# Kernel tuning notes

Hardware: AMD Instinct MI355X
Metric: run time of the kernel (lower is better)

## Reference

```python
import jax, jax.numpy as jnp
import numpy as np
import math

NM = 1024
NH = 16
ND = NM // NH
B, L = 4, 1024


def setup_inputs() -> dict:
    key = jax.random.key(0)
    ks = jax.random.split(key, 11)
    s = 1.0 / math.sqrt(NM)
    return {
        "x": jax.random.normal(ks[0], (B, L, NM), dtype=jnp.float32),
        "mask": jax.random.randint(ks[1], (B, L, L), 0, 2, dtype=jnp.int32),
        "Wq": jax.random.normal(ks[2], (NM, NM), dtype=jnp.float32) * s,
        "bq": jax.random.normal(ks[3], (NM,), dtype=jnp.float32) * 0.01,
        "Wk": jax.random.normal(ks[4], (NM, NM), dtype=jnp.float32) * s,
        "bk": jax.random.normal(ks[5], (NM,), dtype=jnp.float32) * 0.01,
        "Wv": jax.random.normal(ks[6], (NM, NM), dtype=jnp.float32) * s,
        "bv": jax.random.normal(ks[7], (NM,), dtype=jnp.float32) * 0.01,
        "Wo": jax.random.normal(ks[8], (NM, NM), dtype=jnp.float32) * s,
        "bo": jax.random.normal(ks[9], (NM,), dtype=jnp.float32) * 0.01,
    }


def reference(x, mask, Wq, bq, Wk, bk, Wv, bv, Wo, bo):
    nB, nL, _ = x.shape
    m = mask.astype(x.dtype)  # [B,L,L]
    # QKV projections (torch Linear: y = x @ W.T + b)
    q = (x @ Wq.T + bq).reshape(nB, nL, NH, ND)
    k = (x @ Wk.T + bk).reshape(nB, nL, NH, ND)
    v = (x @ Wv.T + bv).reshape(nB, nL, NH, ND)
    # scaled dot product; NOTE: module scales by 1/sqrt(nM), not 1/sqrt(nD)
    scores = jnp.einsum("bqhd,bkhd->bhqk", q, k) / math.sqrt(NM)
    # additive/multiplicative padding mask: S*mask - (1-mask)*1e9
    mb = m[:, None, :, :]  # broadcast over heads [B,1,L,L]
    scores = scores * mb - (1.0 - mb) * 1e9
    attn = jax.nn.softmax(scores, axis=-1)
    ctx = jnp.einsum("bhqk,bkhd->bqhd", attn, v).reshape(nB, nL, NM)
    out = ctx @ Wo.T + bo
    return out
```

## Files before the change

kernel.cpp:

```cpp
#include <hip/hip_runtime.h>

typedef unsigned short u16;
typedef unsigned int   u32;
typedef unsigned long long u64;
typedef __attribute__((ext_vector_type(8))) short    short8;
typedef __attribute__((ext_vector_type(4))) float    floatx4;
typedef __attribute__((ext_vector_type(4))) _Float16 half4v;
typedef __attribute__((ext_vector_type(8))) _Float16 half8v;

#define NM 1024
#define NH 16
#define ND 64
#define BB 4
#define LL 1024
#define MM (BB*LL)

__device__ __forceinline__ u16 f2bf(float f) {
  union { float f; u32 u; } c; c.f = f;
  u32 u = c.u;
  return (u16)((u + 0x7fffu + ((u >> 16) & 1u)) >> 16);
}

__device__ __forceinline__ void cstore(u16* p, float v)  { *p = f2bf(v); }
__device__ __forceinline__ void cstore(float* p, float v){ *p = v; }

__device__ __forceinline__ void load_lds16(const void* g, void* l) {
  __builtin_amdgcn_global_load_lds((const __attribute__((address_space(1))) u32*)g,
                                   (__attribute__((address_space(3))) u32*)l,
                                   16, 0, 0);
}

__device__ __forceinline__ int vperm(int K) {
  return (K & ~31) | (((K >> 2) & 3) << 3) | (((K >> 4) & 1) << 2) | (K & 3);
}

__global__ void conv_all(const float* __restrict__ x,  const float* __restrict__ Wq,
                         const float* __restrict__ Wk, const float* __restrict__ Wv,
                         const float* __restrict__ Wo, const int* __restrict__ m,
                         u16* __restrict__ xb, u16* __restrict__ wcat,
                         u16* __restrict__ wob, u32* __restrict__ mp) {
  const int y = blockIdx.y;
  const int base = blockIdx.x * 256 + threadIdx.x;
  if (y == 5) {
    const int lane = threadIdx.x & 63;
    #pragma unroll
    for (int t = 0; t < 16; t++) {
      int i = base + t * 262144;
      int v = m[i];
      u64 bits = __ballot(v != 0);
      if (lane == 0) {
        mp[(i >> 5) + 0] = (u32)bits;
        mp[(i >> 5) + 1] = (u32)(bits >> 32);
      }
    }
    return;
  }
  const float* src; u16* dst;
  if      (y == 0) { src = x;  dst = xb; }
  else if (y == 1) { src = Wq; dst = wcat; }
  else if (y == 2) { src = Wk; dst = wcat + NM * NM; }
  else if (y == 3) { src = Wv; dst = wcat + 2 * NM * NM; }
  else             { src = Wo; dst = wob; }
  const int nrep = (y == 0) ? 4 : 1;
  for (int t = 0; t < nrep; t++) {
    int i = (base + t * 262144) * 4;
    float4 v = *(const float4*)(src + i);
    ushort4 o;
    o.x = f2bf(v.x); o.y = f2bf(v.y); o.z = f2bf(v.z); o.w = f2bf(v.w);
    *(ushort4*)(dst + i) = o;
  }
}

template<int TM, int TN, typename OUT_T, bool TRANS_Z2>
__global__ __launch_bounds__(256)
void gemm_bt_kernel(const u16* __restrict__ A,
                    const u16* __restrict__ Ball,
                    const float* __restrict__ b0, const float* __restrict__ b1,
                    const float* __restrict__ b2,
                    OUT_T* __restrict__ Call,
                    _Float16* __restrict__ VTout)
{
  constexpr int K = 1024, N = 1024;
  constexpr int NI = TM / 32, NJ = TN / 32;
  constexpr int CH = (TM + TN) / 16;
  const int z = blockIdx.z;
  const u16* Bm = Ball + (size_t)z * N * K;
  const float* bias = (z == 0) ? b0 : ((z == 1) ? b1 : b2);
  OUT_T* C = Call + (size_t)z * MM * N;

  __shared__ u16 S[(TM + TN) * 32];
  u16* As = S;
  u16* Bs = S + TM * 32;

  const int tid = threadIdx.x;
  const int w = tid >> 6, lane = tid & 63, lane15 = lane & 15, quad = lane >> 4;
  const int row0 = blockIdx.x * TM, col0 = blockIdx.y * TN;
  const int wm = (w >> 1) * (TM / 2), wn = (w & 1) * (TN / 2);
  const int sr = lane >> 2, sc = (lane & 3) * 8;

  floatx4 acc[NI][NJ];
  const floatx4 zero = {0.f, 0.f, 0.f, 0.f};
  #pragma unroll
  for (int i = 0; i < NI; i++)
    #pragma unroll
    for (int j = 0; j < NJ; j++) acc[i][j] = zero;

  for (int kk = 0; kk < K; kk += 32) {
    __syncthreads();
    #pragma unroll
    for (int c = 0; c < CH / 4; c++) {
      int g = w * (CH / 4) + c;
      const u16* src;
      if (g * 16 < TM) src = A  + (size_t)(row0 + g * 16 + sr) * K + kk + sc;
      else             src = Bm + (size_t)(col0 + (g * 16 - TM) + sr) * K + kk + sc;
      load_lds16(src, &S[g * 512]);
    }
    __syncthreads();

    short8 af[NI], bf[NJ];
    #pragma unroll
    for (int i = 0; i < NI; i++)
      af[i] = *(short8*)&As[(wm + i * 16 + lane15) * 32 + quad * 8];
    #pragma unroll
    for (int j = 0; j < NJ; j++)
      bf[j] = *(short8*)&Bs[(wn + j * 16 + lane15) * 32 + quad * 8];
    #pragma unroll
    for (int i = 0; i < NI; i++)
      #pragma unroll
      for (int j = 0; j < NJ; j++)
        acc[i][j] = __builtin_amdgcn_mfma_f32_16x16x32_bf16(af[i], bf[j], acc[i][j], 0, 0, 0);
  }

  #pragma unroll
  for (int i = 0; i < NI; i++) {
    #pragma unroll
    for (int j = 0; j < NJ; j++) {
      int col = col0 + wn + j * 16 + lane15;
      float bv = bias[col];
      if (TRANS_Z2 && z == 2) {
        int row = row0 + wm + i * 16 + quad * 4;
        int Kk = row & (LL - 1), bb = row & ~(LL - 1);
        int o = vperm(Kk);
        half4v hv;
        hv.x = (_Float16)(acc[i][j][0] + bv);
        hv.y = (_Float16)(acc[i][j][1] + bv);
        hv.z = (_Float16)(acc[i][j][2] + bv);
        hv.w = (_Float16)(acc[i][j][3] + bv);
        *(half4v*)&VTout[(size_t)col * MM + bb + o] = hv;
      } else {
        #pragma unroll
        for (int r = 0; r < 4; r++) {
          int row = row0 + wm + i * 16 + quad * 4 + r;
          cstore(&C[(size_t)row * N + col], acc[i][j][r] + bv);
        }
      }
    }
  }
}

__global__ __launch_bounds__(256, 2)
void attn_kernel(const u16* __restrict__ Q, const u16* __restrict__ K,
                 const _Float16* __restrict__ VT, const u32* __restrict__ mp,
                 u16* __restrict__ CTX)
{
  __shared__ u16      Ks[2 * 128 * 32];
  __shared__ _Float16 Vs[64 * 128];

  const int tid = threadIdx.x;
  const int w = tid >> 6, lane = tid & 63, lane15 = lane & 15, quad = lane >> 4;
  const int qb = blockIdx.x * 128, bh = blockIdx.y;
  const int b = bh >> 4, h = bh & 15;
  const size_t kvbase = (size_t)(b * LL) * NM + h * ND;
  const size_t vtbase = (size_t)(h * ND) * MM + (size_t)b * LL;
  const float scale = 0.03125f;

  int q0g[2];
  q0g[0] = qb + w * 16;
  q0g[1] = qb + 64 + w * 16;

  short8 aq[2][2];
  #pragma unroll
  for (int g = 0; g < 2; g++) {
    const u16* qp = Q + (size_t)(b * LL + q0g[g] + lane15) * NM + h * ND + quad * 8;
    aq[g][0] = *(const short8*)(qp);
    aq[g][1] = *(const short8*)(qp + 32);
  }

  const int ksrow = lane >> 2;
  const int kscg  = (lane & 3) ^ (ksrow & 3);
  const int vsd   = lane >> 4;
  const int vscg  = (lane & 15);

  const floatx4 zero = {0.f, 0.f, 0.f, 0.f};
  floatx4 o_acc[2][4] = {{zero, zero, zero, zero}, {zero, zero, zero, zero}};
  float lsum[2] = {0.f, 0.f};

  const u32* mrow0 = mp + (size_t)(b * LL + q0g[0] + lane15) * 32;
  const u32* mrow1 = mp + (size_t)(b * LL + q0g[1] + lane15) * 32;

  #pragma unroll 1
  for (int kt = 0; kt < 8; kt++) {
    const int k0 = kt * 128;

    __syncthreads();
    #pragma unroll
    for (int t = 0; t < 4; t++) {
      int n = w * 4 + t;
      int s = n & 1, r0 = (n >> 1) * 16;
      int row = r0 + ksrow;
      load_lds16(K + kvbase + (size_t)(k0 + row) * NM + s * 32 + kscg * 8,
                 &Ks[n * 512]);
    }
    #pragma unroll
    for (int t = 0; t < 4; t++) {
      int n = w * 4 + t;
      int d = n * 4 + vsd;
      int cg = vscg ^ (d & 15);
      load_lds16(VT + vtbase + (size_t)d * MM + k0 + cg * 8, &Vs[n * 512]);
    }
    __syncthreads();

    #pragma unroll
    for (int g = 0; g < 2; g++) {
      const u32* mrow = g ? mrow1 : mrow0;
      const uint4 m4 = *(const uint4*)(mrow + kt * 4);

      half4v pf[8];
      #pragma unroll
      for (int j = 0; j < 8; j++) {
        const int ch = (quad ^ (lane15 & 3)) * 8;
        const int kbase = j * 1024 + lane15 * 32 + ch;
        const short8 kf0 = *(const short8*)&Ks[kbase];
        const short8 kf1 = *(const short8*)&Ks[kbase + 512];
        floatx4 sT = zero;
        sT = __builtin_amdgcn_mfma_f32_16x16x32_bf16(kf0, aq[g][0], sT, 0, 0, 0);
        sT = __builtin_amdgcn_mfma_f32_16x16x32_bf16(kf1, aq[g][1], sT, 0, 0, 0);
        const u32 mw = (j & 2) ? ((j & 4) ? m4.w : m4.y) : ((j & 4) ? m4.z : m4.x);
        const int sh = (j & 1) * 16 + quad * 4;
        float p[4];
        #pragma unroll
        for (int r = 0; r < 4; r++) {
          float e = __expf(sT[r] * scale);
          p[r] = ((mw >> (sh + r)) & 1u) ? e : 0.f;
          lsum[g] += p[r];
        }
        const auto lo = __builtin_amdgcn_cvt_pkrtz(p[0], p[1]);
        const auto hi = __builtin_amdgcn_cvt_pkrtz(p[2], p[3]);
        half4v pj;
        pj.x = (_Float16)lo.x; pj.y = (_Float16)lo.y;
        pj.z = (_Float16)hi.x; pj.w = (_Float16)hi.y;
        pf[j] = pj;
      }

      #pragma unroll
      for (int jd = 0; jd < 4; jd++) {
        const int d = jd * 16 + lane15;
        #pragma unroll
        for (int j2 = 0; j2 < 4; j2++) {
          const int cidx = (j2 * 4 + quad) ^ (d & 15);
          const half8v vv = *(const half8v*)&Vs[d * 128 + cidx * 8];
          const half4v vlo = __builtin_shufflevector(vv, vv, 0, 1, 2, 3);
          const half4v vhi = __builtin_shufflevector(vv, vv, 4, 5, 6, 7);
          o_acc[g][jd] = __builtin_amdgcn_mfma_f32_16x16x16f16(vlo, pf[2 * j2],     o_acc[g][jd], 0, 0, 0);
          o_acc[g][jd] = __builtin_amdgcn_mfma_f32_16x16x16f16(vhi, pf[2 * j2 + 1], o_acc[g][jd], 0, 0, 0);
        }
      }
    }
  }

  #pragma unroll
  for (int g = 0; g < 2; g++) {
    float ls = lsum[g];
    ls += __shfl_xor(ls, 16);
    ls += __shfl_xor(ls, 32);
    const float inv = 1.0f / ls;
    const size_t obase = (size_t)(b * LL + q0g[g] + lane15) * NM + h * ND;
    #pragma unroll
    for (int jd = 0; jd < 4; jd++) {
      ushort4 o;
      o.x = f2bf(o_acc[g][jd][0] * inv);
      o.y = f2bf(o_acc[g][jd][1] * inv);
      o.z = f2bf(o_acc[g][jd][2] * inv);
      o.w = f2bf(o_acc[g][jd][3] * inv);
      *(ushort4*)(CTX + obase + jd * 16 + quad * 4) = o;
    }
  }
}

extern "C" void kernel_launch(void* const* d_in, const int* in_sizes, int n_in,
                              void* d_out, int out_size, void* d_ws, size_t ws_size,
                              hipStream_t stream) {
  const float* x  = (const float*)d_in[0];
  const int*   mk = (const int*)  d_in[1];
  const float* Wq = (const float*)d_in[2]; const float* bq = (const float*)d_in[3];
  const float* Wk = (const float*)d_in[4]; const float* bk = (const float*)d_in[5];
  const float* Wv = (const float*)d_in[6]; const float* bv = (const float*)d_in[7];
  const float* Wo = (const float*)d_in[8]; const float* bo = (const float*)d_in[9];
  float* out = (float*)d_out;

  char* ws = (char*)d_ws;
  u16* xb        = (u16*)(ws);
  u16* Wcat      = (u16*)(ws + ((size_t)8  << 20));
  u16* Wob       = (u16*)(ws + ((size_t)14 << 20));
  u16* QKb       = (u16*)(ws + ((size_t)16 << 20));
  _Float16* VT   = (_Float16*)(ws + ((size_t)32 << 20));
  u16* CTX       = (u16*)(ws + ((size_t)40 << 20));
  u32* mp        = (u32*)(ws + ((size_t)48 << 20));

  conv_all<<<dim3(1024, 6), 256, 0, stream>>>(x, Wq, Wk, Wv, Wo, mk,
                                              xb, Wcat, Wob, mp);

  gemm_bt_kernel<128, 128, u16, true><<<dim3(32, 8, 3), 256, 0, stream>>>(
      xb, Wcat, bq, bk, bv, QKb, VT);

  attn_kernel<<<dim3(8, 64), 256, 0, stream>>>(
      QKb, QKb + (size_t)MM * NM, VT, mp, CTX);

  gemm_bt_kernel<64, 128, float, false><<<dim3(64, 8, 1), 256, 0, stream>>>(
      CTX, Wob, bo, bo, bo, out, nullptr);
}
```

Before: 198.1 us.

## Double GEMM K-step to 64 and fuse attention query groups with 16x16x32 f16 MFMA

```diff
diff --git a/kernel.cpp b/kernel.cpp
--- a/kernel.cpp
+++ b/kernel.cpp
@@ -82,15 +82,13 @@
 {
   constexpr int K = 1024, N = 1024;
   constexpr int NI = TM / 32, NJ = TN / 32;
-  constexpr int CH = (TM + TN) / 16;
+  constexpr int CH = (TM + TN) / 8;
   const int z = blockIdx.z;
   const u16* Bm = Ball + (size_t)z * N * K;
   const float* bias = (z == 0) ? b0 : ((z == 1) ? b1 : b2);
   OUT_T* C = Call + (size_t)z * MM * N;
 
-  __shared__ u16 S[(TM + TN) * 32];
-  u16* As = S;
-  u16* Bs = S + TM * 32;
+  __shared__ u16 S[(TM + TN) * 64];
 
   const int tid = threadIdx.x;
   const int w = tid >> 6, lane = tid & 63, lane15 = lane & 15, quad = lane >> 4;
@@ -105,30 +103,35 @@
     #pragma unroll
     for (int j = 0; j < NJ; j++) acc[i][j] = zero;
 
-  for (int kk = 0; kk < K; kk += 32) {
+  for (int kk = 0; kk < K; kk += 64) {
     __syncthreads();
     #pragma unroll
     for (int c = 0; c < CH / 4; c++) {
       int g = w * (CH / 4) + c;
+      int rg = g >> 1, s = g & 1;
+      int grow = rg * 16 + sr;
       const u16* src;
-      if (g * 16 < TM) src = A  + (size_t)(row0 + g * 16 + sr) * K + kk + sc;
-      else             src = Bm + (size_t)(col0 + (g * 16 - TM) + sr) * K + kk + sc;
+      if (grow < TM) src = A  + (size_t)(row0 + grow) * K + kk + s * 32 + sc;
+      else           src = Bm + (size_t)(col0 + grow - TM) * K + kk + s * 32 + sc;
       load_lds16(src, &S[g * 512]);
     }
     __syncthreads();
 
-    short8 af[NI], bf[NJ];
-    #pragma unroll
-    for (int i = 0; i < NI; i++)
-      af[i] = *(short8*)&As[(wm + i * 16 + lane15) * 32 + quad * 8];
-    #pragma unroll
-    for (int j = 0; j < NJ; j++)
-      bf[j] = *(short8*)&Bs[(wn + j * 16 + lane15) * 32 + quad * 8];
-    #pragma unroll
-    for (int i = 0; i < NI; i++)
+    #pragma unroll
+    for (int s = 0; s < 2; s++) {
+      short8 af[NI], bf[NJ];
+      #pragma unroll
+      for (int i = 0; i < NI; i++)
+        af[i] = *(short8*)&S[((wm >> 4) + i) * 1024 + s * 512 + lane15 * 32 + quad * 8];
       #pragma unroll
       for (int j = 0; j < NJ; j++)
-        acc[i][j] = __builtin_amdgcn_mfma_f32_16x16x32_bf16(af[i], bf[j], acc[i][j], 0, 0, 0);
+        bf[j] = *(short8*)&S[(((TM + wn) >> 4) + j) * 1024 + s * 512 + lane15 * 32 + quad * 8];
+      #pragma unroll
+      for (int i = 0; i < NI; i++)
+        #pragma unroll
+        for (int j = 0; j < NJ; j++)
+          acc[i][j] = __builtin_amdgcn_mfma_f32_16x16x32_bf16(af[i], bf[j], acc[i][j], 0, 0, 0);
+    }
   }
 
   #pragma unroll
@@ -201,6 +204,9 @@
   #pragma unroll 1
   for (int kt = 0; kt < 8; kt++) {
     const int k0 = kt * 128;
+    uint4 m4g[2];
+    m4g[0] = *(const uint4*)(mrow0 + kt * 4);
+    m4g[1] = *(const uint4*)(mrow1 + kt * 4);
 
     __syncthreads();
     #pragma unroll
@@ -220,27 +226,27 @@
     }
     __syncthreads();
 
-    #pragma unroll
-    for (int g = 0; g < 2; g++) {
-      const u32* mrow = g ? mrow1 : mrow0;
-      const uint4 m4 = *(const uint4*)(mrow + kt * 4);
-
-      half4v pf[8];
-      #pragma unroll
-      for (int j = 0; j < 8; j++) {
-        const int ch = (quad ^ (lane15 & 3)) * 8;
-        const int kbase = j * 1024 + lane15 * 32 + ch;
-        const short8 kf0 = *(const short8*)&Ks[kbase];
-        const short8 kf1 = *(const short8*)&Ks[kbase + 512];
-        floatx4 sT = zero;
-        sT = __builtin_amdgcn_mfma_f32_16x16x32_bf16(kf0, aq[g][0], sT, 0, 0, 0);
-        sT = __builtin_amdgcn_mfma_f32_16x16x32_bf16(kf1, aq[g][1], sT, 0, 0, 0);
+    half4v pf[2][8];
+    #pragma unroll
+    for (int j = 0; j < 8; j++) {
+      const int ch = (quad ^ (lane15 & 3)) * 8;
+      const int kbase = j * 1024 + lane15 * 32 + ch;
+      const short8 kf0 = *(const short8*)&Ks[kbase];
+      const short8 kf1 = *(const short8*)&Ks[kbase + 512];
+      floatx4 sT[2];
+      sT[0] = __builtin_amdgcn_mfma_f32_16x16x32_bf16(kf0, aq[0][0], zero, 0, 0, 0);
+      sT[1] = __builtin_amdgcn_mfma_f32_16x16x32_bf16(kf0, aq[1][0], zero, 0, 0, 0);
+      sT[0] = __builtin_amdgcn_mfma_f32_16x16x32_bf16(kf1, aq[0][1], sT[0], 0, 0, 0);
+      sT[1] = __builtin_amdgcn_mfma_f32_16x16x32_bf16(kf1, aq[1][1], sT[1], 0, 0, 0);
+      const int sh = (j & 1) * 16 + quad * 4;
+      #pragma unroll
+      for (int g = 0; g < 2; g++) {
+        const uint4 m4 = m4g[g];
         const u32 mw = (j & 2) ? ((j & 4) ? m4.w : m4.y) : ((j & 4) ? m4.z : m4.x);
-        const int sh = (j & 1) * 16 + quad * 4;
         float p[4];
         #pragma unroll
         for (int r = 0; r < 4; r++) {
-          float e = __expf(sT[r] * scale);
+          float e = __expf(sT[g][r] * scale);
           p[r] = ((mw >> (sh + r)) & 1u) ? e : 0.f;
           lsum[g] += p[r];
         }
@@ -249,21 +255,23 @@
         half4v pj;
         pj.x = (_Float16)lo.x; pj.y = (_Float16)lo.y;
         pj.z = (_Float16)hi.x; pj.w = (_Float16)hi.y;
-        pf[j] = pj;
+        pf[g][j] = pj;
       }
-
+    }
+
+    #pragma unroll
+    for (int t = 0; t < 4; t++) {
+      const half8v b80 = __builtin_shufflevector(pf[0][2 * t], pf[0][2 * t + 1],
+                                                 0, 1, 2, 3, 4, 5, 6, 7);
+      const half8v b81 = __builtin_shufflevector(pf[1][2 * t], pf[1][2 * t + 1],
+                                                 0, 1, 2, 3, 4, 5, 6, 7);
       #pragma unroll
       for (int jd = 0; jd < 4; jd++) {
         const int d = jd * 16 + lane15;
-        #pragma unroll
-        for (int j2 = 0; j2 < 4; j2++) {
-          const int cidx = (j2 * 4 + quad) ^ (d & 15);
-          const half8v vv = *(const half8v*)&Vs[d * 128 + cidx * 8];
-          const half4v vlo = __builtin_shufflevector(vv, vv, 0, 1, 2, 3);
-          const half4v vhi = __builtin_shufflevector(vv, vv, 4, 5, 6, 7);
-          o_acc[g][jd] = __builtin_amdgcn_mfma_f32_16x16x16f16(vlo, pf[2 * j2],     o_acc[g][jd], 0, 0, 0);
-          o_acc[g][jd] = __builtin_amdgcn_mfma_f32_16x16x16f16(vhi, pf[2 * j2 + 1], o_acc[g][jd], 0, 0, 0);
-        }
+        const int cidx = (t * 4 + quad) ^ (d & 15);
+        const half8v vv = *(const half8v*)&Vs[d * 128 + cidx * 8];
+        o_acc[0][jd] = __builtin_amdgcn_mfma_f32_16x16x32_f16(vv, b80, o_acc[0][jd], 0, 0, 0);
+        o_acc[1][jd] = __builtin_amdgcn_mfma_f32_16x16x32_f16(vv, b81, o_acc[1][jd], 0, 0, 0);
       }
     }
   }
```

New measurement: 204.4 us. 3.1% more time.
